# Optimization experiments

Measured on AMD Instinct MI355X. Metric: run time of the kernel, lower is better.

## Reference

```python
import jax, jax.numpy as jnp
import numpy as np

N_AGENTS = 32
STATE_DIM = 512
LATENT = 16
H = 64  # attention_hidden_dim
N1 = N_AGENTS
N2 = N_AGENTS * (N_AGENTS - 1) // 2
NF = N1 + N2
B = 32768
# pairwise indices, same order as itertools.combinations(range(n), 2)
_PI, _PJ = np.triu_indices(N_AGENTS, k=1)
PI = jnp.asarray(_PI)
PJ = jnp.asarray(_PJ)


def setup_inputs() -> dict:
    key = jax.random.key(0)
    ks = jax.random.split(key, 24)
    s = 0.1  # small init scale (xavier gain 0.5)
    inp = {
        "agent_q_values": jax.random.normal(ks[0], (B, N_AGENTS), jnp.float32),
        "state": jax.random.normal(ks[1], (B, STATE_DIM), jnp.float32),
        "agent_semantics": jax.random.normal(ks[2], (B, N_AGENTS, LATENT), jnp.float32),
        # order-1 shape functions, stacked over N1 functions, weights in [in,out] layout
        "w1_1": jax.random.normal(ks[3], (N1, 1, 8), jnp.float32) * s,
        "b1_1": jnp.zeros((N1, 8), jnp.float32),
        "w2_1": jax.random.normal(ks[4], (N1, 8, 4), jnp.float32) * s,
        "b2_1": jnp.zeros((N1, 4), jnp.float32),
        "w3_1": jax.random.normal(ks[5], (N1, 4, 1), jnp.float32) * s,
        "b3_1": jnp.zeros((N1, 1), jnp.float32),
        # order-2 shape functions, stacked over N2 pairs
        "w1_2": jax.random.normal(ks[6], (N2, 2, 8), jnp.float32) * s,
        "b1_2": jnp.zeros((N2, 8), jnp.float32),
        "w2_2": jax.random.normal(ks[7], (N2, 8, 4), jnp.float32) * s,
        "b2_2": jnp.zeros((N2, 4), jnp.float32),
        "w3_2": jax.random.normal(ks[8], (N2, 4, 1), jnp.float32) * s,
        "b3_2": jnp.zeros((N2, 1), jnp.float32),
        # state encoder
        "ws_w": jax.random.normal(ks[9], (STATE_DIM, H), jnp.float32) * (1.0 / np.sqrt(STATE_DIM)),
        "ws_b": jnp.zeros((H,), jnp.float32),
        # semantic encoder
        "wz_w": jax.random.normal(ks[10], (LATENT * N_AGENTS, H), jnp.float32) * (1.0 / np.sqrt(LATENT * N_AGENTS)),
        "wz_b": jnp.zeros((H,), jnp.float32),
        # attention net
        "wa1_w": jax.random.normal(ks[11], (2 * H, H), jnp.float32) * (1.0 / np.sqrt(2 * H)),
        "wa1_b": jnp.zeros((H,), jnp.float32),
        "wa2_w": jax.random.normal(ks[12], (H, NF), jnp.float32) * (1.0 / np.sqrt(H)),
        "wa2_b": jnp.zeros((NF,), jnp.float32),
        # bias net
        "wb1_w": jax.random.normal(ks[13], (STATE_DIM, H), jnp.float32) * (1.0 / np.sqrt(STATE_DIM)),
        "wb1_b": jnp.zeros((H,), jnp.float32),
        "wb2_w": jax.random.normal(ks[14], (H, 1), jnp.float32) * (1.0 / np.sqrt(H)),
        "wb2_b": jnp.zeros((1,), jnp.float32),
    }
    return inp


def _shape_fns(x, w1, b1, w2, b2, w3, b3):
    # x: [B, N, D_in]; weights stacked over N functions; abs() on weights (monotonicity)
    h = jax.nn.elu(jnp.einsum("bnd,ndh->bnh", x, jnp.abs(w1)) + b1)   # [B,N,8]
    h = jax.nn.elu(jnp.einsum("bnh,nhk->bnk", h, jnp.abs(w2)) + b2)   # [B,N,4]
    f = jnp.einsum("bnk,nk->bn", h, jnp.abs(w3)[:, :, 0]) + b3[:, 0]  # [B,N]
    return f


def reference(agent_q_values, state, agent_semantics,
              w1_1, b1_1, w2_1, b2_1, w3_1, b3_1,
              w1_2, b1_2, w2_2, b2_2, w3_2, b3_2,
              ws_w, ws_b, wz_w, wz_b,
              wa1_w, wa1_b, wa2_w, wa2_b,
              wb1_w, wb1_b, wb2_w, wb2_b):
    q = agent_q_values  # [B, n_agents]
    # order-1 shape functions: input is scalar Q_i
    f1 = _shape_fns(q[:, :, None], w1_1, b1_1, w2_1, b2_1, w3_1, b3_1)   # [B, N1]
    # order-2 shape functions: input is [Q_i, Q_j] per pair
    q_pairs = jnp.stack([q[:, PI], q[:, PJ]], axis=-1)                    # [B, N2, 2]
    f2 = _shape_fns(q_pairs, w1_2, b1_2, w2_2, b2_2, w3_2, b3_2)          # [B, N2]
    shape_outputs = jnp.concatenate([f1, f2], axis=-1)                    # [B, NF]

    state_enc = jax.nn.relu(state @ ws_w + ws_b)                          # [B, H]
    sem_flat = agent_semantics.reshape(agent_semantics.shape[0], -1)      # [B, n*latent]
    sem_enc = jax.nn.relu(sem_flat @ wz_w + wz_b)                         # [B, H]
    combined = jnp.concatenate([state_enc, sem_enc], axis=-1)             # [B, 2H]
    logits = jax.nn.relu(combined @ wa1_w + wa1_b) @ wa2_w + wa2_b        # [B, NF]
    attention_weights = jax.nn.softmax(logits, axis=-1)

    weighted_sum = jnp.sum(attention_weights * shape_outputs, axis=-1, keepdims=True)
    bias = jax.nn.relu(state @ wb1_w + wb1_b) @ wb2_w + wb2_b             # [B, 1]
    q_total = weighted_sum + bias
    return (q_total, attention_weights, shape_outputs)
```

## Files before the change

kernel.cpp:

```cpp
#include <hip/hip_runtime.h>
#include <cstdint>
#include <cstddef>

#define NAG 32
#define N1C 32
#define N2C 496
#define NF 528
#define HD 64
#define SD 512

typedef __attribute__((ext_vector_type(8))) short bf16x8;
typedef __attribute__((ext_vector_type(4))) float f32x4;
#define MFMA16(a, b, c) __builtin_amdgcn_mfma_f32_16x16x32_bf16(a, b, c, 0, 0, 0)

__device__ __forceinline__ unsigned short f2bf(float f) {
    unsigned int u = __float_as_uint(f);
    u += 0x7fffu + ((u >> 16) & 1u);
    return (unsigned short)(u >> 16);
}
__device__ __forceinline__ unsigned int pack2(float a, float b) {
    return (unsigned int)f2bf(a) | ((unsigned int)f2bf(b) << 16);
}
__device__ __forceinline__ float elu_f(float x) {
    return x > 0.f ? x : (__expf(x) - 1.f);
}

#define OFF_WST   0
#define OFF_WB1T  32768
#define OFF_WZT   65536
#define OFF_WA1T  98304
#define OFF_WA2T  106496
#define PREP_TOT  140288

__global__ __launch_bounds__(256) void prep_kernel(
    const float* __restrict__ ws_w, const float* __restrict__ wb1_w,
    const float* __restrict__ wz_w, const float* __restrict__ wa1_w,
    const float* __restrict__ wa2_w, unsigned short* __restrict__ ws)
{
    int i = blockIdx.x * 256 + threadIdx.x;
    if (i >= PREP_TOT) return;
    float v;
    if (i < OFF_WB1T) {
        int j = i - OFF_WST; int n = j >> 9, k = j & 511;
        v = ws_w[k * 64 + n];
    } else if (i < OFF_WZT) {
        int j = i - OFF_WB1T; int n = j >> 9, k = j & 511;
        v = wb1_w[k * 64 + n];
    } else if (i < OFF_WA1T) {
        int j = i - OFF_WZT; int n = j >> 9, k = j & 511;
        v = wz_w[k * 64 + n];
    } else if (i < OFF_WA2T) {
        int j = i - OFF_WA1T; int n = j >> 7, k = j & 127;
        v = wa1_w[k * 64 + n];
    } else {
        int j = i - OFF_WA2T; int n = j >> 6, k = j & 63;
        v = wa2_w[k * NF + n];
    }
    ws[i] = f2bf(v);
}

#define SROWS 64
__global__ __launch_bounds__(576) void shape_kernel(
    const float* __restrict__ q,
    const float* __restrict__ w1_1, const float* __restrict__ b1_1,
    const float* __restrict__ w2_1, const float* __restrict__ b2_1,
    const float* __restrict__ w3_1, const float* __restrict__ b3_1,
    const float* __restrict__ w1_2, const float* __restrict__ b1_2,
    const float* __restrict__ w2_2, const float* __restrict__ b2_2,
    const float* __restrict__ w3_2, const float* __restrict__ b3_2,
    float* __restrict__ shape_out, int B)
{
    __shared__ float qs[SROWS][NAG];

    int tid = threadIdx.x;
    int f = tid;
    bool valid = f < NF;
    int fe = valid ? f : (NF - 1);

    float w1a[8], w1b[8], b1v[8], w2v[32], b2v[4], w3v[4], b3v;
    int pi, pj;
    if (fe < N1C) {
        int n = fe;
        pi = n; pj = n;
        #pragma unroll
        for (int k = 0; k < 8; k++) { w1a[k] = fabsf(w1_1[n*8+k]); w1b[k] = 0.f; b1v[k] = b1_1[n*8+k]; }
        #pragma unroll
        for (int t = 0; t < 32; t++) w2v[t] = fabsf(w2_1[n*32+t]);
        #pragma unroll
        for (int j = 0; j < 4; j++) { b2v[j] = b2_1[n*4+j]; w3v[j] = fabsf(w3_1[n*4+j]); }
        b3v = b3_1[n];
    } else {
        int n = fe - N1C;
        int p = n, i = 0, c = NAG - 1;
        while (p >= c) { p -= c; c--; i++; }
        pi = i; pj = i + 1 + p;
        #pragma unroll
        for (int k = 0; k < 8; k++) { w1a[k] = fabsf(w1_2[n*16+k]); w1b[k] = fabsf(w1_2[n*16+8+k]); b1v[k] = b1_2[n*8+k]; }
        #pragma unroll
        for (int t = 0; t < 32; t++) w2v[t] = fabsf(w2_2[n*32+t]);
        #pragma unroll
        for (int j = 0; j < 4; j++) { b2v[j] = b2_2[n*4+j]; w3v[j] = fabsf(w3_2[n*4+j]); }
        b3v = b3_2[n];
    }

    int row0 = blockIdx.x * SROWS;
    if (tid < 512) {
        float4 v = *(const float4*)&q[(size_t)row0 * NAG + tid * 4];
        *(float4*)&((float*)qs)[tid * 4] = v;
    }
    __syncthreads();

    #pragma unroll 4
    for (int rr = 0; rr < SROWS; rr++) {
        float qi = qs[rr][pi];
        float qj = qs[rr][pj];
        float h1[8];
        #pragma unroll
        for (int k = 0; k < 8; k++) h1[k] = elu_f(w1a[k]*qi + w1b[k]*qj + b1v[k]);
        float h2[4];
        #pragma unroll
        for (int j = 0; j < 4; j++) {
            float a = b2v[j];
            #pragma unroll
            for (int k = 0; k < 8; k++) a += h1[k] * w2v[k*4 + j];
            h2[j] = elu_f(a);
        }
        float fv = b3v;
        #pragma unroll
        for (int j = 0; j < 4; j++) fv += h2[j] * w3v[j];
        if (valid) shape_out[(size_t)(row0 + rr) * NF + f] = fv;
    }
}

#define RB 64
__global__ __launch_bounds__(256, 2) void enc_mfma(
    const float* __restrict__ state,
    const float* __restrict__ sem,
    const unsigned short* __restrict__ wsbuf,
    const float* __restrict__ ws_b, const float* __restrict__ wz_b,
    const float* __restrict__ wa1_b, const float* __restrict__ wa2_b,
    const float* __restrict__ wb1_b, const float* __restrict__ wb2_w,
    const float* __restrict__ wb2_b,
    const float* __restrict__ shape_out,
    float* __restrict__ q_total,
    float* __restrict__ attn_out)
{
    __shared__ unsigned short sA[RB][72];
    __shared__ unsigned short sComb[RB][136];
    __shared__ unsigned short sH[RB][72];

    const unsigned short* wsT  = wsbuf + OFF_WST;
    const unsigned short* wb1T = wsbuf + OFF_WB1T;
    const unsigned short* wzT  = wsbuf + OFF_WZT;
    const unsigned short* wa1T = wsbuf + OFF_WA1T;
    const unsigned short* wa2T = wsbuf + OFF_WA2T;

    int tid  = threadIdx.x;
    int lane = tid & 63;
    int w    = tid >> 6;
    int col  = lane & 15;
    int quad = lane >> 4;
    int r0   = blockIdx.x * RB;
    int rowt = w * 16;

    f32x4 accS[4], accB[4], accZ[4];
    #pragma unroll
    for (int ct = 0; ct < 4; ct++) {
        accS[ct] = (f32x4){0.f,0.f,0.f,0.f};
        accB[ct] = (f32x4){0.f,0.f,0.f,0.f};
        accZ[ct] = (f32x4){0.f,0.f,0.f,0.f};
    }

    for (int chunk = 0; chunk < 8; chunk++) {
        __syncthreads();
        #pragma unroll
        for (int i = 0; i < 4; i++) {
            int idx = i * 256 + tid;
            int sr = idx >> 4;
            int sc = (idx & 15) << 2;
            float4 v = *(const float4*)&state[(size_t)(r0 + sr) * SD + chunk * 64 + sc];
            uint2 p; p.x = pack2(v.x, v.y); p.y = pack2(v.z, v.w);
            *(uint2*)&sA[sr][sc] = p;
        }
        __syncthreads();
        #pragma unroll
        for (int ks = 0; ks < 2; ks++) {
            bf16x8 a = *(const bf16x8*)&sA[rowt + col][ks * 32 + quad * 8];
            int wof = chunk * 64 + ks * 32 + quad * 8;
            #pragma unroll
            for (int ct = 0; ct < 4; ct++) {
                bf16x8 bS = *(const bf16x8*)&wsT [(ct * 16 + col) * SD + wof];
                bf16x8 bB = *(const bf16x8*)&wb1T[(ct * 16 + col) * SD + wof];
                accS[ct] = MFMA16(a, bS, accS[ct]);
                accB[ct] = MFMA16(a, bB, accB[ct]);
            }
        }
    }

    for (int chunk = 0; chunk < 8; chunk++) {
        __syncthreads();
        #pragma unroll
        for (int i = 0; i < 4; i++) {
            int idx = i * 256 + tid;
            int sr = idx >> 4;
            int sc = (idx & 15) << 2;
            float4 v = *(const float4*)&sem[(size_t)(r0 + sr) * SD + chunk * 64 + sc];
            uint2 p; p.x = pack2(v.x, v.y); p.y = pack2(v.z, v.w);
            *(uint2*)&sA[sr][sc] = p;
        }
        __syncthreads();
        #pragma unroll
        for (int ks = 0; ks < 2; ks++) {
            bf16x8 a = *(const bf16x8*)&sA[rowt + col][ks * 32 + quad * 8];
            int wof = chunk * 64 + ks * 32 + quad * 8;
            #pragma unroll
            for (int ct = 0; ct < 4; ct++) {
                bf16x8 bZ = *(const bf16x8*)&wzT[(ct * 16 + col) * SD + wof];
                accZ[ct] = MFMA16(a, bZ, accZ[ct]);
            }
        }
    }

    #pragma unroll
    for (int ct = 0; ct < 4; ct++) {
        float bs = ws_b[ct * 16 + col];
        float bz = wz_b[ct * 16 + col];
        #pragma unroll
        for (int reg = 0; reg < 4; reg++) {
            int rr = rowt + quad * 4 + reg;
            sComb[rr][ct * 16 + col]      = f2bf(fmaxf(accS[ct][reg] + bs, 0.f));
            sComb[rr][64 + ct * 16 + col] = f2bf(fmaxf(accZ[ct][reg] + bz, 0.f));
        }
    }

    float qbv[4];
    #pragma unroll
    for (int reg = 0; reg < 4; reg++) {
        float p = 0.f;
        #pragma unroll
        for (int ct = 0; ct < 4; ct++)
            p += fmaxf(accB[ct][reg] + wb1_b[ct * 16 + col], 0.f) * wb2_w[ct * 16 + col];
        #pragma unroll
        for (int m = 1; m < 16; m <<= 1) p += __shfl_xor(p, m, 64);
        qbv[reg] = p;
    }

    f32x4 accH[4];
    #pragma unroll
    for (int ct = 0; ct < 4; ct++) accH[ct] = (f32x4){0.f,0.f,0.f,0.f};
    #pragma unroll
    for (int ks = 0; ks < 4; ks++) {
        bf16x8 a = *(const bf16x8*)&sComb[rowt + col][ks * 32 + quad * 8];
        #pragma unroll
        for (int ct = 0; ct < 4; ct++) {
            bf16x8 b = *(const bf16x8*)&wa1T[(ct * 16 + col) * 128 + ks * 32 + quad * 8];
            accH[ct] = MFMA16(a, b, accH[ct]);
        }
    }
    #pragma unroll
    for (int ct = 0; ct < 4; ct++) {
        float bh = wa1_b[ct * 16 + col];
        #pragma unroll
        for (int reg = 0; reg < 4; reg++)
            sH[rowt + quad * 4 + reg][ct * 16 + col] = f2bf(fmaxf(accH[ct][reg] + bh, 0.f));
    }

    bf16x8 ha0 = *(const bf16x8*)&sH[rowt + col][quad * 8];
    bf16x8 ha1 = *(const bf16x8*)&sH[rowt + col][32 + quad * 8];

    float sAcc[4] = {0.f,0.f,0.f,0.f};
    float wAcc[4] = {0.f,0.f,0.f,0.f};
    for (int nt = 0; nt < 33; nt++) {
        f32x4 acc = (f32x4){0.f,0.f,0.f,0.f};
        const unsigned short* wp = &wa2T[(nt * 16 + col) * 64 + quad * 8];
        acc = MFMA16(ha0, *(const bf16x8*)wp, acc);
        acc = MFMA16(ha1, *(const bf16x8*)(wp + 32), acc);
        float lb = wa2_b[nt * 16 + col];
        #pragma unroll
        for (int reg = 0; reg < 4; reg++) {
            float e = __expf(acc[reg] + lb);
            sAcc[reg] += e;
            wAcc[reg] += e * shape_out[(size_t)(r0 + rowt + quad * 4 + reg) * NF + nt * 16 + col];
        }
    }
    float inv[4];
    #pragma unroll
    for (int reg = 0; reg < 4; reg++) {
        float s = sAcc[reg], ww = wAcc[reg];
        #pragma unroll
        for (int m = 1; m < 16; m <<= 1) { s += __shfl_xor(s, m, 64); ww += __shfl_xor(ww, m, 64); }
        inv[reg] = 1.f / s;
        if (col == 0)
            q_total[r0 + rowt + quad * 4 + reg] = ww * inv[reg] + qbv[reg] + wb2_b[0];
    }

    for (int nt = 0; nt < 33; nt++) {
        f32x4 acc = (f32x4){0.f,0.f,0.f,0.f};
        const unsigned short* wp = &wa2T[(nt * 16 + col) * 64 + quad * 8];
        acc = MFMA16(ha0, *(const bf16x8*)wp, acc);
        acc = MFMA16(ha1, *(const bf16x8*)(wp + 32), acc);
        float lb = wa2_b[nt * 16 + col];
        #pragma unroll
        for (int reg = 0; reg < 4; reg++) {
            float e = __expf(acc[reg] + lb);
            attn_out[(size_t)(r0 + rowt + quad * 4 + reg) * NF + nt * 16 + col] = e * inv[reg];
        }
    }
}

extern "C" void kernel_launch(void* const* d_in, const int* in_sizes, int n_in,
                              void* d_out, int out_size, void* d_ws, size_t ws_size,
                              hipStream_t stream) {
    const float* q     = (const float*)d_in[0];
    const float* state = (const float*)d_in[1];
    const float* sem   = (const float*)d_in[2];
    const float* w1_1  = (const float*)d_in[3];
    const float* b1_1  = (const float*)d_in[4];
    const float* w2_1  = (const float*)d_in[5];
    const float* b2_1  = (const float*)d_in[6];
    const float* w3_1  = (const float*)d_in[7];
    const float* b3_1  = (const float*)d_in[8];
    const float* w1_2  = (const float*)d_in[9];
    const float* b1_2  = (const float*)d_in[10];
    const float* w2_2  = (const float*)d_in[11];
    const float* b2_2  = (const float*)d_in[12];
    const float* w3_2  = (const float*)d_in[13];
    const float* b3_2  = (const float*)d_in[14];
    const float* ws_w  = (const float*)d_in[15];
    const float* ws_b  = (const float*)d_in[16];
    const float* wz_w  = (const float*)d_in[17];
    const float* wz_b  = (const float*)d_in[18];
    const float* wa1_w = (const float*)d_in[19];
    const float* wa1_b = (const float*)d_in[20];
    const float* wa2_w = (const float*)d_in[21];
    const float* wa2_b = (const float*)d_in[22];
    const float* wb1_w = (const float*)d_in[23];
    const float* wb1_b = (const float*)d_in[24];
    const float* wb2_w = (const float*)d_in[25];
    const float* wb2_b = (const float*)d_in[26];

    int B = in_sizes[0] / NAG;

    float* out_q    = (float*)d_out;
    float* out_attn = out_q + B;
    float* out_shp  = out_attn + (size_t)B * NF;

    unsigned short* wsbuf = (unsigned short*)d_ws;

    prep_kernel<<<(PREP_TOT + 255) / 256, 256, 0, stream>>>(
        ws_w, wb1_w, wz_w, wa1_w, wa2_w, wsbuf);

    shape_kernel<<<B / SROWS, 576, 0, stream>>>(q,
        w1_1, b1_1, w2_1, b2_1, w3_1, b3_1,
        w1_2, b1_2, w2_2, b2_2, w3_2, b3_2,
        out_shp, B);

    enc_mfma<<<B / RB, 256, 0, stream>>>(state, sem, wsbuf,
        ws_b, wz_b, wa1_b, wa2_b, wb1_b, wb2_w, wb2_b,
        out_shp, out_q, out_attn);
}
```

Before: 405.9 us.

## Fuse shape-function MLPs into encoder/attention kernel and drop LDS staging

Merges the separate shape kernel into the MFMA encoder kernel, so each shape value is computed in registers next to its attention logit. This removes the round trip of writing shape_out and reading it back. State and semantic tiles now go straight from global memory into bf16 fragments per wave, with no LDS staging or block barriers, and each wave keeps its own LDS slices. A precomputed pair-index LUT replaces the per-thread while loop. In exchange, per-feature weights are reloaded for every 16-row tile, and register pressure goes up in the fused loop.

```diff
diff --git a/kernel.cpp b/kernel.cpp
--- a/kernel.cpp
+++ b/kernel.cpp
@@ -3,8 +3,6 @@
 #include <cstddef>
 
 #define NAG 32
-#define N1C 32
-#define N2C 496
 #define NF 528
 #define HD 64
 #define SD 512
@@ -21,8 +19,19 @@
 __device__ __forceinline__ unsigned int pack2(float a, float b) {
     return (unsigned int)f2bf(a) | ((unsigned int)f2bf(b) << 16);
 }
+__device__ __forceinline__ bf16x8 pack8(float4 v0, float4 v1) {
+    union { bf16x8 v; unsigned int u[4]; } r;
+    r.u[0] = pack2(v0.x, v0.y);
+    r.u[1] = pack2(v0.z, v0.w);
+    r.u[2] = pack2(v1.x, v1.y);
+    r.u[3] = pack2(v1.z, v1.w);
+    return r.v;
+}
 __device__ __forceinline__ float elu_f(float x) {
     return x > 0.f ? x : (__expf(x) - 1.f);
+}
+__device__ __forceinline__ float4 abs4(float4 v) {
+    return make_float4(fabsf(v.x), fabsf(v.y), fabsf(v.z), fabsf(v.w));
 }
 
 #define OFF_WST   0
@@ -31,13 +40,20 @@
 #define OFF_WA1T  98304
 #define OFF_WA2T  106496
 #define PREP_TOT  140288
+#define OFF_LUT_BYTES (PREP_TOT * 2)
 
 __global__ __launch_bounds__(256) void prep_kernel(
     const float* __restrict__ ws_w, const float* __restrict__ wb1_w,
     const float* __restrict__ wz_w, const float* __restrict__ wa1_w,
-    const float* __restrict__ wa2_w, unsigned short* __restrict__ ws)
+    const float* __restrict__ wa2_w, unsigned short* __restrict__ ws,
+    int* __restrict__ lut)
 {
     int i = blockIdx.x * 256 + threadIdx.x;
+    if (i < 496) {
+        int p = i, a = 0, c = NAG - 1;
+        while (p >= c) { p -= c; c--; a++; }
+        lut[i] = a * 64 + (a + 1 + p);
+    }
     if (i >= PREP_TOT) return;
     float v;
     if (i < OFF_WB1T) {
@@ -59,95 +75,29 @@
     ws[i] = f2bf(v);
 }
 
-#define SROWS 64
-__global__ __launch_bounds__(576) void shape_kernel(
+__global__ __launch_bounds__(256, 2) void fused_kernel(
     const float* __restrict__ q,
+    const float* __restrict__ state,
+    const float* __restrict__ sem,
+    const unsigned short* __restrict__ wsbuf,
+    const int* __restrict__ lut,
     const float* __restrict__ w1_1, const float* __restrict__ b1_1,
     const float* __restrict__ w2_1, const float* __restrict__ b2_1,
     const float* __restrict__ w3_1, const float* __restrict__ b3_1,
     const float* __restrict__ w1_2, const float* __restrict__ b1_2,
     const float* __restrict__ w2_2, const float* __restrict__ b2_2,
     const float* __restrict__ w3_2, const float* __restrict__ b3_2,
-    float* __restrict__ shape_out, int B)
-{
-    __shared__ float qs[SROWS][NAG];
-
-    int tid = threadIdx.x;
-    int f = tid;
-    bool valid = f < NF;
-    int fe = valid ? f : (NF - 1);
-
-    float w1a[8], w1b[8], b1v[8], w2v[32], b2v[4], w3v[4], b3v;
-    int pi, pj;
-    if (fe < N1C) {
-        int n = fe;
-        pi = n; pj = n;
-        #pragma unroll
-        for (int k = 0; k < 8; k++) { w1a[k] = fabsf(w1_1[n*8+k]); w1b[k] = 0.f; b1v[k] = b1_1[n*8+k]; }
-        #pragma unroll
-        for (int t = 0; t < 32; t++) w2v[t] = fabsf(w2_1[n*32+t]);
-        #pragma unroll
-        for (int j = 0; j < 4; j++) { b2v[j] = b2_1[n*4+j]; w3v[j] = fabsf(w3_1[n*4+j]); }
-        b3v = b3_1[n];
-    } else {
-        int n = fe - N1C;
-        int p = n, i = 0, c = NAG - 1;
-        while (p >= c) { p -= c; c--; i++; }
-        pi = i; pj = i + 1 + p;
-        #pragma unroll
-        for (int k = 0; k < 8; k++) { w1a[k] = fabsf(w1_2[n*16+k]); w1b[k] = fabsf(w1_2[n*16+8+k]); b1v[k] = b1_2[n*8+k]; }
-        #pragma unroll
-        for (int t = 0; t < 32; t++) w2v[t] = fabsf(w2_2[n*32+t]);
-        #pragma unroll
-        for (int j = 0; j < 4; j++) { b2v[j] = b2_2[n*4+j]; w3v[j] = fabsf(w3_2[n*4+j]); }
-        b3v = b3_2[n];
-    }
-
-    int row0 = blockIdx.x * SROWS;
-    if (tid < 512) {
-        float4 v = *(const float4*)&q[(size_t)row0 * NAG + tid * 4];
-        *(float4*)&((float*)qs)[tid * 4] = v;
-    }
-    __syncthreads();
-
-    #pragma unroll 4
-    for (int rr = 0; rr < SROWS; rr++) {
-        float qi = qs[rr][pi];
-        float qj = qs[rr][pj];
-        float h1[8];
-        #pragma unroll
-        for (int k = 0; k < 8; k++) h1[k] = elu_f(w1a[k]*qi + w1b[k]*qj + b1v[k]);
-        float h2[4];
-        #pragma unroll
-        for (int j = 0; j < 4; j++) {
-            float a = b2v[j];
-            #pragma unroll
-            for (int k = 0; k < 8; k++) a += h1[k] * w2v[k*4 + j];
-            h2[j] = elu_f(a);
-        }
-        float fv = b3v;
-        #pragma unroll
-        for (int j = 0; j < 4; j++) fv += h2[j] * w3v[j];
-        if (valid) shape_out[(size_t)(row0 + rr) * NF + f] = fv;
-    }
-}
-
-#define RB 64
-__global__ __launch_bounds__(256, 2) void enc_mfma(
-    const float* __restrict__ state,
-    const float* __restrict__ sem,
-    const unsigned short* __restrict__ wsbuf,
     const float* __restrict__ ws_b, const float* __restrict__ wz_b,
     const float* __restrict__ wa1_b, const float* __restrict__ wa2_b,
     const float* __restrict__ wb1_b, const float* __restrict__ wb2_w,
     const float* __restrict__ wb2_b,
-    const float* __restrict__ shape_out,
     float* __restrict__ q_total,
-    float* __restrict__ attn_out)
+    float* __restrict__ attn_out,
+    float* __restrict__ shape_out)
 {
-    __shared__ unsigned short sA[RB][72];
-    __shared__ unsigned short sComb[RB][136];
-    __shared__ unsigned short sH[RB][72];
+    __shared__ float qs[4][16][36];
+    __shared__ unsigned short sComb[4][16][136];
+    __shared__ unsigned short sH[4][16][72];
 
     const unsigned short* wsT  = wsbuf + OFF_WST;
     const unsigned short* wb1T = wsbuf + OFF_WB1T;
@@ -160,8 +110,15 @@
     int w    = tid >> 6;
     int col  = lane & 15;
     int quad = lane >> 4;
-    int r0   = blockIdx.x * RB;
-    int rowt = w * 16;
+    int rw   = blockIdx.x * 64 + w * 16;
+
+    #pragma unroll
+    for (int i = 0; i < 2; i++) {
+        int idx = i * 64 + lane;
+        int r = idx >> 3, c = (idx & 7) * 4;
+        float4 v = *(const float4*)&q[(size_t)(rw + r) * NAG + c];
+        *(float4*)&qs[w][r][c] = v;
+    }
 
     f32x4 accS[4], accB[4], accZ[4];
     #pragma unroll
@@ -171,53 +128,33 @@
         accZ[ct] = (f32x4){0.f,0.f,0.f,0.f};
     }
 
-    for (int chunk = 0; chunk < 8; chunk++) {
-        __syncthreads();
-        #pragma unroll
-        for (int i = 0; i < 4; i++) {
-            int idx = i * 256 + tid;
-            int sr = idx >> 4;
-            int sc = (idx & 15) << 2;
-            float4 v = *(const float4*)&state[(size_t)(r0 + sr) * SD + chunk * 64 + sc];
-            uint2 p; p.x = pack2(v.x, v.y); p.y = pack2(v.z, v.w);
-            *(uint2*)&sA[sr][sc] = p;
-        }
-        __syncthreads();
-        #pragma unroll
-        for (int ks = 0; ks < 2; ks++) {
-            bf16x8 a = *(const bf16x8*)&sA[rowt + col][ks * 32 + quad * 8];
-            int wof = chunk * 64 + ks * 32 + quad * 8;
-            #pragma unroll
-            for (int ct = 0; ct < 4; ct++) {
-                bf16x8 bS = *(const bf16x8*)&wsT [(ct * 16 + col) * SD + wof];
-                bf16x8 bB = *(const bf16x8*)&wb1T[(ct * 16 + col) * SD + wof];
-                accS[ct] = MFMA16(a, bS, accS[ct]);
-                accB[ct] = MFMA16(a, bB, accB[ct]);
-            }
-        }
-    }
-
-    for (int chunk = 0; chunk < 8; chunk++) {
-        __syncthreads();
-        #pragma unroll
-        for (int i = 0; i < 4; i++) {
-            int idx = i * 256 + tid;
-            int sr = idx >> 4;
-            int sc = (idx & 15) << 2;
-            float4 v = *(const float4*)&sem[(size_t)(r0 + sr) * SD + chunk * 64 + sc];
-            uint2 p; p.x = pack2(v.x, v.y); p.y = pack2(v.z, v.w);
-            *(uint2*)&sA[sr][sc] = p;
-        }
-        __syncthreads();
-        #pragma unroll
-        for (int ks = 0; ks < 2; ks++) {
-            bf16x8 a = *(const bf16x8*)&sA[rowt + col][ks * 32 + quad * 8];
-            int wof = chunk * 64 + ks * 32 + quad * 8;
-            #pragma unroll
-            for (int ct = 0; ct < 4; ct++) {
-                bf16x8 bZ = *(const bf16x8*)&wzT[(ct * 16 + col) * SD + wof];
-                accZ[ct] = MFMA16(a, bZ, accZ[ct]);
-            }
+    const float* As = state + (size_t)(rw + col) * SD + quad * 8;
+    const float* Az = sem   + (size_t)(rw + col) * SD + quad * 8;
+
+    #pragma unroll 4
+    for (int ks = 0; ks < 16; ks++) {
+        float4 v0 = *(const float4*)(As + ks * 32);
+        float4 v1 = *(const float4*)(As + ks * 32 + 4);
+        bf16x8 a = pack8(v0, v1);
+        int wof = ks * 32 + quad * 8;
+        #pragma unroll
+        for (int ct = 0; ct < 4; ct++) {
+            bf16x8 bS = *(const bf16x8*)&wsT [(ct * 16 + col) * SD + wof];
+            bf16x8 bB = *(const bf16x8*)&wb1T[(ct * 16 + col) * SD + wof];
+            accS[ct] = MFMA16(a, bS, accS[ct]);
+            accB[ct] = MFMA16(a, bB, accB[ct]);
+        }
+    }
+    #pragma unroll 4
+    for (int ks = 0; ks < 16; ks++) {
+        float4 v0 = *(const float4*)(Az + ks * 32);
+        float4 v1 = *(const float4*)(Az + ks * 32 + 4);
+        bf16x8 a = pack8(v0, v1);
+        int wof = ks * 32 + quad * 8;
+        #pragma unroll
+        for (int ct = 0; ct < 4; ct++) {
+            bf16x8 bZ = *(const bf16x8*)&wzT[(ct * 16 + col) * SD + wof];
+            accZ[ct] = MFMA16(a, bZ, accZ[ct]);
         }
     }
 
@@ -227,9 +164,9 @@
         float bz = wz_b[ct * 16 + col];
         #pragma unroll
         for (int reg = 0; reg < 4; reg++) {
-            int rr = rowt + quad * 4 + reg;
-            sComb[rr][ct * 16 + col]      = f2bf(fmaxf(accS[ct][reg] + bs, 0.f));
-            sComb[rr][64 + ct * 16 + col] = f2bf(fmaxf(accZ[ct][reg] + bz, 0.f));
+            int rr = quad * 4 + reg;
+            sComb[w][rr][ct * 16 + col]      = f2bf(fmaxf(accS[ct][reg] + bs, 0.f));
+            sComb[w][rr][64 + ct * 16 + col] = f2bf(fmaxf(accZ[ct][reg] + bz, 0.f));
         }
     }
 
@@ -250,7 +187,7 @@
     for (int ct = 0; ct < 4; ct++) accH[ct] = (f32x4){0.f,0.f,0.f,0.f};
     #pragma unroll
     for (int ks = 0; ks < 4; ks++) {
-        bf16x8 a = *(const bf16x8*)&sComb[rowt + col][ks * 32 + quad * 8];
+        bf16x8 a = *(const bf16x8*)&sComb[w][col][ks * 32 + quad * 8];
         #pragma unroll
         for (int ct = 0; ct < 4; ct++) {
             bf16x8 b = *(const bf16x8*)&wa1T[(ct * 16 + col) * 128 + ks * 32 + quad * 8];
@@ -262,28 +199,91 @@
         float bh = wa1_b[ct * 16 + col];
         #pragma unroll
         for (int reg = 0; reg < 4; reg++)
-            sH[rowt + quad * 4 + reg][ct * 16 + col] = f2bf(fmaxf(accH[ct][reg] + bh, 0.f));
-    }
-
-    bf16x8 ha0 = *(const bf16x8*)&sH[rowt + col][quad * 8];
-    bf16x8 ha1 = *(const bf16x8*)&sH[rowt + col][32 + quad * 8];
+            sH[w][quad * 4 + reg][ct * 16 + col] = f2bf(fmaxf(accH[ct][reg] + bh, 0.f));
+    }
+
+    bf16x8 ha0 = *(const bf16x8*)&sH[w][col][quad * 8];
+    bf16x8 ha1 = *(const bf16x8*)&sH[w][col][32 + quad * 8];
+
+    union F8  { float4 v[2]; float f[8];  };
+    union F32 { float4 v[8]; float f[32]; };
+    union F4  { float4 v;    float f[4];  };
 
     float sAcc[4] = {0.f,0.f,0.f,0.f};
     float wAcc[4] = {0.f,0.f,0.f,0.f};
+
+    #pragma unroll 1
     for (int nt = 0; nt < 33; nt++) {
         f32x4 acc = (f32x4){0.f,0.f,0.f,0.f};
         const unsigned short* wp = &wa2T[(nt * 16 + col) * 64 + quad * 8];
         acc = MFMA16(ha0, *(const bf16x8*)wp, acc);
         acc = MFMA16(ha1, *(const bf16x8*)(wp + 32), acc);
         float lb = wa2_b[nt * 16 + col];
+
+        int f = nt * 16 + col;
+        F8 W1A, W1B, B1; F32 W2; F4 B2, W3; float b3v;
+        int pi, pj;
+        if (nt < 2) {
+            int n = f;
+            pi = n; pj = n;
+            const float4* p = (const float4*)(w1_1 + n * 8);
+            W1A.v[0] = abs4(p[0]); W1A.v[1] = abs4(p[1]);
+            W1B.v[0] = make_float4(0.f,0.f,0.f,0.f); W1B.v[1] = W1B.v[0];
+            const float4* pb = (const float4*)(b1_1 + n * 8);
+            B1.v[0] = pb[0]; B1.v[1] = pb[1];
+            const float4* p2 = (const float4*)(w2_1 + n * 32);
+            #pragma unroll
+            for (int t = 0; t < 8; t++) W2.v[t] = abs4(p2[t]);
+            B2.v = *(const float4*)(b2_1 + n * 4);
+            W3.v = abs4(*(const float4*)(w3_1 + n * 4));
+            b3v = b3_1[n];
+        } else {
+            int n = f - 32;
+            int pk = lut[n];
+            pi = pk >> 6; pj = pk & 63;
+            const float4* p = (const float4*)(w1_2 + n * 16);
+            W1A.v[0] = abs4(p[0]); W1A.v[1] = abs4(p[1]);
+            W1B.v[0] = abs4(p[2]); W1B.v[1] = abs4(p[3]);
+            const float4* pb = (const float4*)(b1_2 + n * 8);
+            B1.v[0] = pb[0]; B1.v[1] = pb[1];
+            const float4* p2 = (const float4*)(w2_2 + n * 32);
+            #pragma unroll
+            for (int t = 0; t < 8; t++) W2.v[t] = abs4(p2[t]);
+            B2.v = *(const float4*)(b2_2 + n * 4);
+            W3.v = abs4(*(const float4*)(w3_2 + n * 4));
+            b3v = b3_2[n];
+        }
+
         #pragma unroll
         for (int reg = 0; reg < 4; reg++) {
+            int rl = quad * 4 + reg;
+            float qi = qs[w][rl][pi];
+            float qj = qs[w][rl][pj];
+            float h1[8];
+            #pragma unroll
+            for (int k = 0; k < 8; k++)
+                h1[k] = elu_f(W1A.f[k] * qi + W1B.f[k] * qj + B1.f[k]);
+            float h2[4];
+            #pragma unroll
+            for (int j = 0; j < 4; j++) {
+                float a2 = B2.f[j];
+                #pragma unroll
+                for (int k = 0; k < 8; k++) a2 += h1[k] * W2.f[k * 4 + j];
+                h2[j] = elu_f(a2);
+            }
+            float fv = b3v;
+            #pragma unroll
+            for (int j = 0; j < 4; j++) fv += h2[j] * W3.f[j];
+
+            shape_out[(size_t)(rw + rl) * NF + f] = fv;
             float e = __expf(acc[reg] + lb);
             sAcc[reg] += e;
-            wAcc[reg] += e * shape_out[(size_t)(r0 + rowt + quad * 4 + reg) * NF + nt * 16 + col];
-        }
-    }
+            wAcc[reg] += e * fv;
+        }
+    }
+
     float inv[4];
+    float wb2b0 = wb2_b[0];
     #pragma unroll
     for (int reg = 0; reg < 4; reg++) {
         float s = sAcc[reg], ww = wAcc[reg];
@@ -291,9 +291,10 @@
         for (int m = 1; m < 16; m <<= 1) { s += __shfl_xor(s, m, 64); ww += __shfl_xor(ww, m, 64); }
         inv[reg] = 1.f / s;
         if (col == 0)
-            q_total[r0 + rowt + quad * 4 + reg] = ww * inv[reg] + qbv[reg] + wb2_b[0];
-    }
-
+            q_total[rw + quad * 4 + reg] = ww * inv[reg] + qbv[reg] + wb2b0;
+    }
+
+    #pragma unroll 1
     for (int nt = 0; nt < 33; nt++) {
         f32x4 acc = (f32x4){0.f,0.f,0.f,0.f};
         const unsigned short* wp = &wa2T[(nt * 16 + col) * 64 + quad * 8];
@@ -303,7 +304,7 @@
         #pragma unroll
         for (int reg = 0; reg < 4; reg++) {
             float e = __expf(acc[reg] + lb);
-            attn_out[(size_t)(r0 + rowt + quad * 4 + reg) * NF + nt * 16 + col] = e * inv[reg];
+            attn_out[(size_t)(rw + quad * 4 + reg) * NF + nt * 16 + col] = e * inv[reg];
         }
     }
 }
@@ -346,16 +347,14 @@
     float* out_shp  = out_attn + (size_t)B * NF;
 
     unsigned short* wsbuf = (unsigned short*)d_ws;
+    int* lut = (int*)((char*)d_ws + OFF_LUT_BYTES);
 
     prep_kernel<<<(PREP_TOT + 255) / 256, 256, 0, stream>>>(
-        ws_w, wb1_w, wz_w, wa1_w, wa2_w, wsbuf);
-
-    shape_kernel<<<B / SROWS, 576, 0, stream>>>(q,
+        ws_w, wb1_w, wz_w, wa1_w, wa2_w, wsbuf, lut);
+
+    fused_kernel<<<B / 64, 256, 0, stream>>>(q, state, sem, wsbuf, lut,
         w1_1, b1_1, w2_1, b2_1, w3_1, b3_1,
         w1_2, b1_2, w2_2, b2_2, w3_2, b3_2,
-        out_shp, B);
-
-    enc_mfma<<<B / RB, 256, 0, stream>>>(state, sem, wsbuf,
         ws_b, wz_b, wa1_b, wa2_b, wb1_b, wb2_w, wb2_b,
-        out_shp, out_q, out_attn);
-}
+        out_q, out_attn, out_shp);
+}
```

Result: slower. 435.1 us (+7.2%).
